# Optimization experiments

Hardware: AMD Instinct MI355X
Metric: run time of the kernel (lower is better)

The kernel has to match this reference:

```python
import jax, jax.numpy as jnp
import numpy as np

EPS = 1e-5
SLOPE = 0.2


def knn_feature(x, k):
    # x: (B,N,C) -> (B,N,k,2C) edge features: concat(neighbor - center, center)
    xx = jnp.sum(x * x, axis=-1)                      # (B,N)
    inner = jnp.einsum('bnc,bmc->bnm', x, x)          # (B,N,N)
    pair = 2.0 * inner - xx[:, :, None] - xx[:, None, :]  # negative squared dist
    idx = jax.lax.top_k(pair, k)[1]                   # (B,N,k) nearest neighbors
    nbr = jax.vmap(lambda xb, ib: xb[ib])(x, idx)     # (B,N,k,C) gather
    ctr = jnp.broadcast_to(x[:, :, None, :], nbr.shape)
    return jnp.concatenate([nbr - ctr, ctr], axis=-1)


def conv_bn_lrelu(h, w, g, b):
    # 1x1 conv == pointwise matmul; BN in training mode (batch stats, biased var)
    h = jnp.einsum('bnkc,oc->bnko', h, w)
    m = jnp.mean(h, axis=(0, 1, 2))
    v = jnp.mean(jnp.square(h - m), axis=(0, 1, 2))
    h = g * (h - m) * jax.lax.rsqrt(v + EPS) + b
    return jnp.where(h >= 0, h, SLOPE * h)


def setup_inputs() -> dict:
    key = jax.random.key(0)
    B, N, C, K, H, O = 4, 4096, 3, 20, 64, 64
    ks = jax.random.split(key, 10)
    x = jax.random.normal(ks[0], (B, N, C), dtype=jnp.float32)
    def w(kk, o, i):
        return jax.random.normal(kk, (o, i), dtype=jnp.float32) * (1.0 / np.sqrt(i))
    return {
        'x': x,
        'w1': w(ks[1], H, 2 * C),
        'w2': w(ks[2], H, H),
        'w3': w(ks[3], H, H),
        'w4': w(ks[4], H, 2 * H),
        'w5': w(ks[5], H, H),
        'w6': w(ks[6], H, H),
        'w7': w(ks[7], H, 2 * H),
        'w8': w(ks[8], H, H),
        'w9': w(ks[9], O, H),
        'gamma': jnp.ones((9, H), dtype=jnp.float32),
        'beta': jnp.zeros((9, H), dtype=jnp.float32),
        'k': 20,
    }


def reference(x, w1, w2, w3, w4, w5, w6, w7, w8, w9, gamma, beta, k):
    h = knn_feature(x, k)                      # (B,N,k,6)
    h = conv_bn_lrelu(h, w1, gamma[0], beta[0])
    h = conv_bn_lrelu(h, w2, gamma[1], beta[1])
    h = conv_bn_lrelu(h, w3, gamma[2], beta[2])
    x1 = jnp.max(h, axis=2)                    # (B,N,64)
    h = knn_feature(x1, k)                     # (B,N,k,128)
    h = conv_bn_lrelu(h, w4, gamma[3], beta[3])
    h = conv_bn_lrelu(h, w5, gamma[4], beta[4])
    h = conv_bn_lrelu(h, w6, gamma[5], beta[5])
    x2 = jnp.max(h, axis=2)                    # (B,N,64)
    h = knn_feature(x2, k)                     # (B,N,k,128)
    h = conv_bn_lrelu(h, w7, gamma[6], beta[6])
    h = conv_bn_lrelu(h, w8, gamma[7], beta[7])
    h = conv_bn_lrelu(h, w9, gamma[8], beta[8])
    x3 = jnp.max(h, axis=2)                    # (B,N,out_features)
    return x3
```

## Files before the change

kernel.cpp:

```cpp
#include <hip/hip_runtime.h>

namespace {

constexpr int Bc   = 4;
constexpr int Nc   = 4096;
constexpr int Kc   = 20;
constexpr int BNc  = Bc * Nc;
constexpr int PIXc = BNc * Kc;
constexpr float  NEGINF = -3.0e38f;
constexpr double EPSD   = (double)1e-5f;

template<int C>
__device__ __forceinline__ float fma_dot(const float* __restrict__ a,
                                         const float* __restrict__ b) {
    float acc = 0.f;
#pragma unroll
    for (int c = 0; c < C; ++c) acc = __builtin_fmaf(a[c], b[c], acc);
    return acc;
}

template<int C>
__global__ __launch_bounds__(256)
void compute_xx_xla(const float* __restrict__ X, float* __restrict__ xxf) {
    int i = blockIdx.x * 256 + threadIdx.x;
    if (i >= BNc) return;
    const float* xp = X + (size_t)i * C;
    if constexpr (C == 3) {
        const float q0 = __fmul_rn(xp[0], xp[0]);
        const float q1 = __fmul_rn(xp[1], xp[1]);
        const float q2 = __fmul_rn(xp[2], xp[2]);
        xxf[i] = __fadd_rn(__fadd_rn(q0, q1), q2);
    } else {
        float acc[16];
#pragma unroll
        for (int l = 0; l < 16; ++l) acc[l] = 0.f;
#pragma unroll
        for (int blk = 0; blk < 4; ++blk)
#pragma unroll
            for (int l = 0; l < 16; ++l)
                acc[l] = __fadd_rn(acc[l], __fmul_rn(xp[blk * 16 + l], xp[blk * 16 + l]));
        float a8[8];
#pragma unroll
        for (int l = 0; l < 8; ++l) a8[l] = __fadd_rn(acc[l], acc[l + 8]);
        float a4[4];
#pragma unroll
        for (int l = 0; l < 4; ++l) a4[l] = __fadd_rn(a8[l], a8[l + 4]);
        xxf[i] = __fadd_rn(__fadd_rn(a4[0], a4[2]), __fadd_rn(a4[1], a4[3]));
    }
}

template<int C>
__global__ __launch_bounds__(256)
void pair_tile(const float* __restrict__ X, const float* __restrict__ xxf,
               float* __restrict__ S, int b) {
    constexpr int P = C + 1;
    __shared__ float sxn[64 * P], sxm[64 * P];
    __shared__ float sxxn[64], sxxm[64];
    const int tid = threadIdx.x;
    const int tn  = blockIdx.x >> 6;
    const int tm  = blockIdx.x & 63;
    const float* Xn = X + ((size_t)b * Nc + tn * 64) * C;
    const float* Xm = X + ((size_t)b * Nc + tm * 64) * C;
    for (int f = tid; f < 64 * C; f += 256) {
        const int row = f / C, c = f - row * C;
        sxn[row * P + c] = Xn[f];
        sxm[row * P + c] = Xm[f];
    }
    if (tid < 64)        sxxn[tid]      = xxf[b * Nc + tn * 64 + tid];
    else if (tid < 128)  sxxm[tid - 64] = xxf[b * Nc + tm * 64 + (tid - 64)];
    __syncthreads();

    const int rn0 = (tid >> 4) * 4;
    const int rm0 = (tid & 15) * 4;
    float a00=0,a01=0,a02=0,a03=0, a10=0,a11=0,a12=0,a13=0;
    float a20=0,a21=0,a22=0,a23=0, a30=0,a31=0,a32=0,a33=0;
#pragma unroll 4
    for (int c = 0; c < C; ++c) {
        const float n0 = sxn[(rn0    ) * P + c];
        const float n1 = sxn[(rn0 + 1) * P + c];
        const float n2 = sxn[(rn0 + 2) * P + c];
        const float n3 = sxn[(rn0 + 3) * P + c];
        const float m0 = sxm[(rm0    ) * P + c];
        const float m1 = sxm[(rm0 + 1) * P + c];
        const float m2 = sxm[(rm0 + 2) * P + c];
        const float m3 = sxm[(rm0 + 3) * P + c];
        a00 = __builtin_fmaf(n0, m0, a00); a01 = __builtin_fmaf(n0, m1, a01);
        a02 = __builtin_fmaf(n0, m2, a02); a03 = __builtin_fmaf(n0, m3, a03);
        a10 = __builtin_fmaf(n1, m0, a10); a11 = __builtin_fmaf(n1, m1, a11);
        a12 = __builtin_fmaf(n1, m2, a12); a13 = __builtin_fmaf(n1, m3, a13);
        a20 = __builtin_fmaf(n2, m0, a20); a21 = __builtin_fmaf(n2, m1, a21);
        a22 = __builtin_fmaf(n2, m2, a22); a23 = __builtin_fmaf(n2, m3, a23);
        a30 = __builtin_fmaf(n3, m0, a30); a31 = __builtin_fmaf(n3, m1, a31);
        a32 = __builtin_fmaf(n3, m2, a32); a33 = __builtin_fmaf(n3, m3, a33);
    }
    const float xm0 = sxxm[rm0], xm1 = sxxm[rm0 + 1], xm2 = sxxm[rm0 + 2], xm3 = sxxm[rm0 + 3];
#define PAIR_ROW(i, r0, r1, r2, r3)                                                     \
    {                                                                                   \
        const float xn_ = sxxn[rn0 + i];                                                \
        float4 v;                                                                       \
        v.x = __fsub_rn(__fsub_rn(__fmul_rn(2.0f, r0), xn_), xm0);                      \
        v.y = __fsub_rn(__fsub_rn(__fmul_rn(2.0f, r1), xn_), xm1);                      \
        v.z = __fsub_rn(__fsub_rn(__fmul_rn(2.0f, r2), xn_), xm2);                      \
        v.w = __fsub_rn(__fsub_rn(__fmul_rn(2.0f, r3), xn_), xm3);                      \
        *(float4*)&S[(size_t)(tn * 64 + rn0 + i) * Nc + tm * 64 + rm0] = v;             \
    }
    PAIR_ROW(0, a00, a01, a02, a03)
    PAIR_ROW(1, a10, a11, a12, a13)
    PAIR_ROW(2, a20, a21, a22, a23)
    PAIR_ROW(3, a30, a31, a32, a33)
#undef PAIR_ROW
}

__global__ __launch_bounds__(256)
void brute_select(const float* __restrict__ S, int* __restrict__ knnIdx, int b) {
    const int lane = threadIdx.x & 63;
    const int wv   = threadIdx.x >> 6;
    const int n    = blockIdx.x * 4 + wv;
    const float* Sr = S + (size_t)n * Nc;
    float v[64];
#pragma unroll
    for (int j = 0; j < 64; ++j) v[j] = Sr[j * 64 + lane];
    int* outp = knnIdx + ((size_t)b * Nc + n) * Kc;
    for (int round = 0; round < Kc; ++round) {
        float bv = NEGINF; int bi = 0x7fffffff;
#pragma unroll
        for (int j = 0; j < 64; ++j) {
            const int mi = j * 64 + lane;
            const bool better = (v[j] > bv) || (v[j] == bv && mi < bi);
            bv = better ? v[j] : bv;
            bi = better ? mi : bi;
        }
#pragma unroll
        for (int s = 1; s < 64; s <<= 1) {
            const float ov = __shfl_xor(bv, s);
            const int   oi = __shfl_xor(bi, s);
            const bool better = (ov > bv) || (ov == bv && oi < bi);
            bv = better ? ov : bv;
            bi = better ? oi : bi;
        }
        if (lane == 0) outp[round] = bi;
#pragma unroll
        for (int j = 0; j < 64; ++j)
            if (j == (bi >> 6) && (bi & 63) == lane) v[j] = NEGINF;
    }
}

__device__ __forceinline__ float bn_lrelu_np(float hv, float m, float r,
                                             float g, float bb) {
    float t = __fsub_rn(hv, m);
    t = __fmul_rn(g, t);
    t = __fmul_rn(t, r);
    t = __fadd_rn(t, bb);
    return t >= 0.f ? t : __fmul_rn(0.2f, t);
}

template<int CIN>
__global__ __launch_bounds__(256)
void edge_conv_fma(const float* __restrict__ X, const int* __restrict__ knnIdx,
                   const float* __restrict__ W, float* __restrict__ h) {
    constexpr int F = 2 * CIN;
    __shared__ float sw[64 * F];
    const int tid = threadIdx.x;
    for (int f = tid; f < 64 * F; f += 256) sw[f] = W[f];
    __syncthreads();
    const int p  = blockIdx.x * 256 + tid;
    const int bn = p / Kc;
    const int b  = bn >> 12;
    const int j  = knnIdx[p];
    const float* cp  = X + (size_t)bn * CIN;
    const float* npt = X + ((size_t)(b << 12) + j) * CIN;
    float feat[F];
#pragma unroll
    for (int c = 0; c < CIN; ++c) {
        const float ct = cp[c];
        feat[c]       = __fsub_rn(npt[c], ct);
        feat[CIN + c] = ct;
    }
    float* hp = h + (size_t)p * 64;
#pragma unroll
    for (int o = 0; o < 64; ++o) hp[o] = fma_dot<F>(feat, &sw[o * F]);
}

__global__ __launch_bounds__(256)
void hidden_conv_fma(float* __restrict__ h, const float* __restrict__ W,
                     const float* __restrict__ mr, const float* __restrict__ g,
                     const float* __restrict__ bt) {
    __shared__ float sw[4096];
    __shared__ float sm[64], sr[64], sg[64], sb[64];
    const int tid = threadIdx.x;
    for (int f = tid; f < 4096; f += 256) sw[f] = W[f];
    if (tid < 64) { sm[tid] = mr[tid]; sr[tid] = mr[64 + tid]; sg[tid] = g[tid]; sb[tid] = bt[tid]; }
    __syncthreads();
    const int p = blockIdx.x * 256 + tid;
    float* hp = h + (size_t)p * 64;
    float in[64];
#pragma unroll
    for (int c = 0; c < 64; ++c) in[c] = bn_lrelu_np(hp[c], sm[c], sr[c], sg[c], sb[c]);
    float hf[64];
#pragma unroll
    for (int o = 0; o < 64; ++o) hf[o] = fma_dot<64>(in, &sw[o * 64]);
#pragma unroll
    for (int o = 0; o < 64; o += 4)
        *(float4*)&hp[o] = make_float4(hf[o], hf[o+1], hf[o+2], hf[o+3]);
}

__global__ __launch_bounds__(256)
void maxk_np(const float* __restrict__ h, const float* __restrict__ mr,
             const float* __restrict__ g, const float* __restrict__ bt,
             float* __restrict__ out) {
    const int i  = blockIdx.x * 256 + threadIdx.x;
    const int o  = i & 63;
    const int bn = i >> 6;
    const float m = mr[o], r = mr[64 + o], gg = g[o], bb = bt[o];
    const float* hp = h + (size_t)bn * Kc * 64 + o;
    float mx = NEGINF;
#pragma unroll
    for (int k = 0; k < Kc; ++k) mx = fmaxf(mx, bn_lrelu_np(hp[k * 64], m, r, gg, bb));
    out[i] = mx;
}

__global__ __launch_bounds__(256)
void stats64(const float* __restrict__ h, double* __restrict__ stats) {
    __shared__ double sp[4 * 128];
    const int tid = threadIdx.x, o = tid & 63, w = tid >> 6;
    double s1 = 0.0, s2 = 0.0;
    for (int p = blockIdx.x * 4 + w; p < PIXc; p += 4096) {
        const double d = (double)h[(size_t)p * 64 + o];
        s1 += d; s2 += d * d;
    }
    sp[w * 128 + o]      = s1;
    sp[w * 128 + 64 + o] = s2;
    __syncthreads();
    if (tid < 128) {
        const double s = sp[tid] + sp[128 + tid] + sp[256 + tid] + sp[384 + tid];
        atomicAdd(&stats[tid], s);
    }
}

__global__ void finalize_f(const double* __restrict__ stats, float* __restrict__ mr) {
    const int o = threadIdx.x;
    const double inv  = 1.0 / (double)PIXc;
    const double mean = stats[o] * inv;
    const double var  = stats[64 + o] * inv - mean * mean;
    mr[o]      = (float)mean;
    mr[64 + o] = (float)(1.0 / sqrt(var + EPSD));
}

}

extern "C" void kernel_launch(void* const* d_in, const int* in_sizes, int n_in,
                              void* d_out, int out_size, void* d_ws, size_t ws_size,
                              hipStream_t stream) {
    (void)in_sizes; (void)n_in; (void)out_size; (void)ws_size;
    const float* x     = (const float*)d_in[0];
    const float* w[9]  = {(const float*)d_in[1], (const float*)d_in[2], (const float*)d_in[3],
                          (const float*)d_in[4], (const float*)d_in[5], (const float*)d_in[6],
                          (const float*)d_in[7], (const float*)d_in[8], (const float*)d_in[9]};
    const float* gamma = (const float*)d_in[10];
    const float* beta  = (const float*)d_in[11];
    float* out = (float*)d_out;

    double* statsD = (double*)d_ws;
    float*  mr     = (float*)(statsD + 9 * 128);
    float*  xxf    = mr + 9 * 128;
    int*  knnIdx   = (int*)(xxf + BNc);
    float* x1      = (float*)(knnIdx + PIXc);
    float* x2      = x1 + (size_t)BNc * 64;
    float* h       = x2 + (size_t)BNc * 64;
    float* S       = h;

    hipMemsetAsync(statsD, 0, 9 * 128 * sizeof(double), stream);

#define BN_STATS(L) \
    stats64<<<1024, 256, 0, stream>>>(h, statsD + (L) * 128); \
    finalize_f<<<1, 64, 0, stream>>>(statsD + (L) * 128, mr + (L) * 128)

    compute_xx_xla<3><<<64, 256, 0, stream>>>(x, xxf);
    for (int b = 0; b < Bc; ++b) {
        pair_tile<3><<<4096, 256, 0, stream>>>(x, xxf, S, b);
        brute_select<<<1024, 256, 0, stream>>>(S, knnIdx, b);
    }
    edge_conv_fma<3><<<1280, 256, 0, stream>>>(x, knnIdx, w[0], h);
    BN_STATS(0);
    hidden_conv_fma<<<1280, 256, 0, stream>>>(h, w[1], mr + 0 * 128, gamma + 0 * 64, beta + 0 * 64);
    BN_STATS(1);
    hidden_conv_fma<<<1280, 256, 0, stream>>>(h, w[2], mr + 1 * 128, gamma + 1 * 64, beta + 1 * 64);
    BN_STATS(2);
    maxk_np<<<4096, 256, 0, stream>>>(h, mr + 2 * 128, gamma + 2 * 64, beta + 2 * 64, x1);

    compute_xx_xla<64><<<64, 256, 0, stream>>>(x1, xxf);
    for (int b = 0; b < Bc; ++b) {
        pair_tile<64><<<4096, 256, 0, stream>>>(x1, xxf, S, b);
        brute_select<<<1024, 256, 0, stream>>>(S, knnIdx, b);
    }
    edge_conv_fma<64><<<1280, 256, 0, stream>>>(x1, knnIdx, w[3], h);
    BN_STATS(3);
    hidden_conv_fma<<<1280, 256, 0, stream>>>(h, w[4], mr + 3 * 128, gamma + 3 * 64, beta + 3 * 64);
    BN_STATS(4);
    hidden_conv_fma<<<1280, 256, 0, stream>>>(h, w[5], mr + 4 * 128, gamma + 4 * 64, beta + 4 * 64);
    BN_STATS(5);
    maxk_np<<<4096, 256, 0, stream>>>(h, mr + 5 * 128, gamma + 5 * 64, beta + 5 * 64, x2);

    compute_xx_xla<64><<<64, 256, 0, stream>>>(x2, xxf);
    for (int b = 0; b < Bc; ++b) {
        pair_tile<64><<<4096, 256, 0, stream>>>(x2, xxf, S, b);
        brute_select<<<1024, 256, 0, stream>>>(S, knnIdx, b);
    }
    edge_conv_fma<64><<<1280, 256, 0, stream>>>(x2, knnIdx, w[6], h);
    BN_STATS(6);
    hidden_conv_fma<<<1280, 256, 0, stream>>>(h, w[7], mr + 6 * 128, gamma + 6 * 64, beta + 6 * 64);
    BN_STATS(7);
    hidden_conv_fma<<<1280, 256, 0, stream>>>(h, w[8], mr + 7 * 128, gamma + 7 * 64, beta + 7 * 64);
    BN_STATS(8);
    maxk_np<<<4096, 256, 0, stream>>>(h, mr + 8 * 128, gamma + 8 * 64, beta + 8 * 64, out);
#undef BN_STATS
}
```

Baseline: 4.104 ms.

## Replace per-pixel conv kernels with shared-memory register-tiled matmul kernels

The pointwise conv layers now use a cooperative tile scheme. Each block stages a tile of 64 (or 32) pixels' input features and a transposed weight matrix in shared memory, and each thread computes a 4x4 (or 4x2) register tile of outputs. The old kernels had one thread per pixel, each holding 64-wide input and output arrays in registers, reading uncoalesced per-pixel rows and producing strided writes. The new scheme is meant to cut register pressure, coalesce global loads and stores, and reuse operands from registers. The cost is extra shared-memory staging and a synchronisation per block.

```diff
diff --git a/kernel.cpp b/kernel.cpp
--- a/kernel.cpp
+++ b/kernel.cpp
@@ -9,15 +9,6 @@
 constexpr int PIXc = BNc * Kc;
 constexpr float  NEGINF = -3.0e38f;
 constexpr double EPSD   = (double)1e-5f;
-
-template<int C>
-__device__ __forceinline__ float fma_dot(const float* __restrict__ a,
-                                         const float* __restrict__ b) {
-    float acc = 0.f;
-#pragma unroll
-    for (int c = 0; c < C; ++c) acc = __builtin_fmaf(a[c], b[c], acc);
-    return acc;
-}
 
 template<int C>
 __global__ __launch_bounds__(256)
@@ -154,54 +145,111 @@
     return t >= 0.f ? t : __fmul_rn(0.2f, t);
 }
 
-template<int CIN>
-__global__ __launch_bounds__(256)
-void edge_conv_fma(const float* __restrict__ X, const int* __restrict__ knnIdx,
-                   const float* __restrict__ W, float* __restrict__ h) {
-    constexpr int F = 2 * CIN;
-    __shared__ float sw[64 * F];
+template<int CIN, int TP, int PM, int OM>
+__global__ __launch_bounds__(256)
+void edge_conv_tile(const float* __restrict__ X, const int* __restrict__ knn,
+                    const float* __restrict__ W, float* __restrict__ h) {
+    constexpr int F  = 2 * CIN;
+    constexpr int PW = (F & 3) ? (F + 4 - (F & 3)) : (F + 4);
+    __shared__ float sA[TP * PW];
+    __shared__ float sWT[F * 68];
     const int tid = threadIdx.x;
-    for (int f = tid; f < 64 * F; f += 256) sw[f] = W[f];
+    for (int f = tid; f < 64 * F; f += 256) {
+        const int o = f / F, c = f - o * F;
+        sWT[c * 68 + o] = W[f];
+    }
+    const int pix0 = blockIdx.x * TP;
+    for (int f = tid; f < TP * F; f += 256) {
+        const int pix = f / F, c = f - pix * F;
+        const int p  = pix0 + pix;
+        const int bn = p / Kc;
+        const int b  = bn >> 12;
+        const int j  = knn[p];
+        float v;
+        if (c < CIN) v = __fsub_rn(X[((size_t)(b << 12) + j) * CIN + c],
+                                   X[(size_t)bn * CIN + c]);
+        else         v = X[(size_t)bn * CIN + (c - CIN)];
+        sA[pix * PW + c] = v;
+    }
     __syncthreads();
-    const int p  = blockIdx.x * 256 + tid;
-    const int bn = p / Kc;
-    const int b  = bn >> 12;
-    const int j  = knnIdx[p];
-    const float* cp  = X + (size_t)bn * CIN;
-    const float* npt = X + ((size_t)(b << 12) + j) * CIN;
-    float feat[F];
-#pragma unroll
-    for (int c = 0; c < CIN; ++c) {
-        const float ct = cp[c];
-        feat[c]       = __fsub_rn(npt[c], ct);
-        feat[CIN + c] = ct;
-    }
-    float* hp = h + (size_t)p * 64;
-#pragma unroll
-    for (int o = 0; o < 64; ++o) hp[o] = fma_dot<F>(feat, &sw[o * F]);
-}
-
-__global__ __launch_bounds__(256)
-void hidden_conv_fma(float* __restrict__ h, const float* __restrict__ W,
-                     const float* __restrict__ mr, const float* __restrict__ g,
-                     const float* __restrict__ bt) {
-    __shared__ float sw[4096];
-    __shared__ float sm[64], sr[64], sg[64], sb[64];
+
+    constexpr int TX = 64 / OM;
+    const int ty = tid / TX, tx = tid - ty * TX;
+    const int p0 = ty * PM, o0 = tx * OM;
+    float acc[PM][OM];
+#pragma unroll
+    for (int i = 0; i < PM; ++i)
+#pragma unroll
+        for (int j = 0; j < OM; ++j) acc[i][j] = 0.f;
+#pragma unroll 2
+    for (int c = 0; c < F; ++c) {
+        float av[PM], wv[OM];
+#pragma unroll
+        for (int i = 0; i < PM; ++i) av[i] = sA[(p0 + i) * PW + c];
+#pragma unroll
+        for (int j = 0; j < OM; ++j) wv[j] = sWT[c * 68 + o0 + j];
+#pragma unroll
+        for (int i = 0; i < PM; ++i)
+#pragma unroll
+            for (int j = 0; j < OM; ++j)
+                acc[i][j] = __builtin_fmaf(av[i], wv[j], acc[i][j]);
+    }
+#pragma unroll
+    for (int i = 0; i < PM; ++i) {
+        float* dst = &h[(size_t)(pix0 + p0 + i) * 64 + o0];
+        if constexpr (OM == 4)
+            *(float4*)dst = make_float4(acc[i][0], acc[i][1], acc[i][2], acc[i][3]);
+        else
+            *(float2*)dst = make_float2(acc[i][0], acc[i][1]);
+    }
+}
+
+__global__ __launch_bounds__(256)
+void hidden_conv_tile(float* __restrict__ h, const float* __restrict__ W,
+                      const float* __restrict__ mr, const float* __restrict__ g,
+                      const float* __restrict__ bt) {
+    __shared__ float sA[64 * 65];
+    __shared__ float sWT[64 * 68];
     const int tid = threadIdx.x;
-    for (int f = tid; f < 4096; f += 256) sw[f] = W[f];
-    if (tid < 64) { sm[tid] = mr[tid]; sr[tid] = mr[64 + tid]; sg[tid] = g[tid]; sb[tid] = bt[tid]; }
+    for (int f = tid; f < 4096; f += 256) {
+        const int o = f >> 6, c = f & 63;
+        sWT[c * 68 + o] = W[f];
+    }
+    const size_t pix0 = (size_t)blockIdx.x * 64;
+    for (int f = tid; f < 4096; f += 256) {
+        const int pix = f >> 6, c = f & 63;
+        const float hv = h[(pix0 + pix) * 64 + c];
+        sA[pix * 65 + c] = bn_lrelu_np(hv, mr[c], mr[64 + c], g[c], bt[c]);
+    }
     __syncthreads();
-    const int p = blockIdx.x * 256 + tid;
-    float* hp = h + (size_t)p * 64;
-    float in[64];
-#pragma unroll
-    for (int c = 0; c < 64; ++c) in[c] = bn_lrelu_np(hp[c], sm[c], sr[c], sg[c], sb[c]);
-    float hf[64];
-#pragma unroll
-    for (int o = 0; o < 64; ++o) hf[o] = fma_dot<64>(in, &sw[o * 64]);
-#pragma unroll
-    for (int o = 0; o < 64; o += 4)
-        *(float4*)&hp[o] = make_float4(hf[o], hf[o+1], hf[o+2], hf[o+3]);
+
+    const int ty = tid >> 4, tx = tid & 15;
+    const int p0 = ty * 4, o0 = tx * 4;
+    float acc[4][4];
+#pragma unroll
+    for (int i = 0; i < 4; ++i)
+#pragma unroll
+        for (int j = 0; j < 4; ++j) acc[i][j] = 0.f;
+#pragma unroll 4
+    for (int c = 0; c < 64; ++c) {
+        const float4 wv = *(const float4*)&sWT[c * 68 + o0];
+        const float a0 = sA[(p0    ) * 65 + c];
+        const float a1 = sA[(p0 + 1) * 65 + c];
+        const float a2 = sA[(p0 + 2) * 65 + c];
+        const float a3 = sA[(p0 + 3) * 65 + c];
+        acc[0][0] = __builtin_fmaf(a0, wv.x, acc[0][0]); acc[0][1] = __builtin_fmaf(a0, wv.y, acc[0][1]);
+        acc[0][2] = __builtin_fmaf(a0, wv.z, acc[0][2]); acc[0][3] = __builtin_fmaf(a0, wv.w, acc[0][3]);
+        acc[1][0] = __builtin_fmaf(a1, wv.x, acc[1][0]); acc[1][1] = __builtin_fmaf(a1, wv.y, acc[1][1]);
+        acc[1][2] = __builtin_fmaf(a1, wv.z, acc[1][2]); acc[1][3] = __builtin_fmaf(a1, wv.w, acc[1][3]);
+        acc[2][0] = __builtin_fmaf(a2, wv.x, acc[2][0]); acc[2][1] = __builtin_fmaf(a2, wv.y, acc[2][1]);
+        acc[2][2] = __builtin_fmaf(a2, wv.z, acc[2][2]); acc[2][3] = __builtin_fmaf(a2, wv.w, acc[2][3]);
+        acc[3][0] = __builtin_fmaf(a3, wv.x, acc[3][0]); acc[3][1] = __builtin_fmaf(a3, wv.y, acc[3][1]);
+        acc[3][2] = __builtin_fmaf(a3, wv.z, acc[3][2]); acc[3][3] = __builtin_fmaf(a3, wv.w, acc[3][3]);
+    }
+#pragma unroll
+    for (int i = 0; i < 4; ++i)
+        *(float4*)&h[(pix0 + p0 + i) * 64 + o0] =
+            make_float4(acc[i][0], acc[i][1], acc[i][2], acc[i][3]);
 }
 
 __global__ __launch_bounds__(256)
@@ -280,11 +328,11 @@
         pair_tile<3><<<4096, 256, 0, stream>>>(x, xxf, S, b);
         brute_select<<<1024, 256, 0, stream>>>(S, knnIdx, b);
     }
-    edge_conv_fma<3><<<1280, 256, 0, stream>>>(x, knnIdx, w[0], h);
+    edge_conv_tile<3, 64, 4, 4><<<PIXc / 64, 256, 0, stream>>>(x, knnIdx, w[0], h);
     BN_STATS(0);
-    hidden_conv_fma<<<1280, 256, 0, stream>>>(h, w[1], mr + 0 * 128, gamma + 0 * 64, beta + 0 * 64);
+    hidden_conv_tile<<<PIXc / 64, 256, 0, stream>>>(h, w[1], mr + 0 * 128, gamma + 0 * 64, beta + 0 * 64);
     BN_STATS(1);
-    hidden_conv_fma<<<1280, 256, 0, stream>>>(h, w[2], mr + 1 * 128, gamma + 1 * 64, beta + 1 * 64);
+    hidden_conv_tile<<<PIXc / 64, 256, 0, stream>>>(h, w[2], mr + 1 * 128, gamma + 1 * 64, beta + 1 * 64);
     BN_STATS(2);
     maxk_np<<<4096, 256, 0, stream>>>(h, mr + 2 * 128, gamma + 2 * 64, beta + 2 * 64, x1);
 
@@ -293,11 +341,11 @@
         pair_tile<64><<<4096, 256, 0, stream>>>(x1, xxf, S, b);
         brute_select<<<1024, 256, 0, stream>>>(S, knnIdx, b);
     }
-    edge_conv_fma<64><<<1280, 256, 0, stream>>>(x1, knnIdx, w[3], h);
+    edge_conv_tile<64, 32, 4, 2><<<PIXc / 32, 256, 0, stream>>>(x1, knnIdx, w[3], h);
     BN_STATS(3);
-    hidden_conv_fma<<<1280, 256, 0, stream>>>(h, w[4], mr + 3 * 128, gamma + 3 * 64, beta + 3 * 64);
+    hidden_conv_tile<<<PIXc / 64, 256, 0, stream>>>(h, w[4], mr + 3 * 128, gamma + 3 * 64, beta + 3 * 64);
     BN_STATS(4);
-    hidden_conv_fma<<<1280, 256, 0, stream>>>(h, w[5], mr + 4 * 128, gamma + 4 * 64, beta + 4 * 64);
+    hidden_conv_tile<<<PIXc / 64, 256, 0, stream>>>(h, w[5], mr + 4 * 128, gamma + 4 * 64, beta + 4 * 64);
     BN_STATS(5);
     maxk_np<<<4096, 256, 0, stream>>>(h, mr + 5 * 128, gamma + 5 * 64, beta + 5 * 64, x2);
 
@@ -306,11 +354,11 @@
         pair_tile<64><<<4096, 256, 0, stream>>>(x2, xxf, S, b);
         brute_select<<<1024, 256, 0, stream>>>(S, knnIdx, b);
     }
-    edge_conv_fma<64><<<1280, 256, 0, stream>>>(x2, knnIdx, w[6], h);
+    edge_conv_tile<64, 32, 4, 2><<<PIXc / 32, 256, 0, stream>>>(x2, knnIdx, w[6], h);
     BN_STATS(6);
-    hidden_conv_fma<<<1280, 256, 0, stream>>>(h, w[7], mr + 6 * 128, gamma + 6 * 64, beta + 6 * 64);
+    hidden_conv_tile<<<PIXc / 64, 256, 0, stream>>>(h, w[7], mr + 6 * 128, gamma + 6 * 64, beta + 6 * 64);
     BN_STATS(7);
-    hidden_conv_fma<<<1280, 256, 0, stream>>>(h, w[8], mr + 7 * 128, gamma + 7 * 64, beta + 7 * 64);
+    hidden_conv_tile<<<PIXc / 64, 256, 0, stream>>>(h, w[8], mr + 7 * 128, gamma + 7 * 64, beta + 7 * 64);
     BN_STATS(8);
     maxk_np<<<4096, 256, 0, stream>>>(h, mr + 8 * 128, gamma + 8 * 64, beta + 8 * 64, out);
 #undef BN_STATS
```

Result: faster. 3.478 ms (-15.2%).
